# Optimization experiments

Hardware: AMD Instinct MI355X
Metric: run time of the kernel (lower is better)

Reference implementation:

```python
import jax, jax.numpy as jnp
import numpy as np

B, S, D = 16, 1024, 768          # batch, seq_len, in_features
NS, MAXW = 256, 8                # num_spans, max span width (fixed for jit)
V, C = 128, 6                    # num_vertexes, max corefs per vertex
R = 512                          # num_max_rels_per_example
REL, HID, DIS = 97, 384, 20      # relation_num, hidden_dim, dis_size
NEG = -1e30


def setup_inputs() -> dict:
    key = jax.random.key(0)
    ks = jax.random.split(key, 14)
    sentence_repr = jax.random.normal(ks[0], (B, S, D), jnp.float32)
    starts = jax.random.randint(ks[1], (B, NS), 0, S - MAXW)
    widths = jax.random.randint(ks[2], (B, NS), 0, MAXW)
    entity_span_indices = jnp.stack([starts, starts + widths], axis=-1)  # (B,NS,2), start<=end
    entity_span_indices_mask = jax.random.randint(ks[3], (B, NS), 0, 2)
    vertex_indices = jax.random.randint(ks[4], (B, V, C), 0, NS)
    vertex_indices_mask = jax.random.randint(ks[5], (B, V, C), 0, 2)
    head_tail_indices = jax.random.randint(ks[6], (B, R, 2), 0, V)
    relation_mask = jax.random.randint(ks[7], (B, R), 0, 2)
    dis_h_2_t = jax.random.randint(ks[8], (B, R), 0, 20)
    dis_t_2_h = jax.random.randint(ks[9], (B, R), 0, 20)
    dis_embed = jax.random.normal(ks[10], (20, DIS), jnp.float32) * 0.02
    dis_embed = dis_embed.at[10].set(0.0)  # padding_idx=10
    fin = D + DIS                      # final_in_features with distance
    in_proj = 2 * fin + D              # concat [head+dis, tail+dis, head*tail]
    W1 = jax.random.normal(ks[11], (in_proj, HID), jnp.float32) / np.float32(np.sqrt(in_proj))
    W2 = jax.random.normal(ks[12], (HID, REL), jnp.float32) / np.float32(np.sqrt(HID))
    b2 = jnp.zeros((REL,), jnp.float32)
    return dict(sentence_repr=sentence_repr, entity_span_indices=entity_span_indices,
                entity_span_indices_mask=entity_span_indices_mask,
                vertex_indices=vertex_indices, vertex_indices_mask=vertex_indices_mask,
                head_tail_indices=head_tail_indices, relation_mask=relation_mask,
                dis_h_2_t=dis_h_2_t, dis_t_2_h=dis_t_2_h,
                dis_embed=dis_embed, W1=W1, W2=W2, b2=b2)


def reference(sentence_repr, entity_span_indices, entity_span_indices_mask,
              vertex_indices, vertex_indices_mask, head_tail_indices,
              relation_mask, dis_h_2_t, dis_t_2_h, dis_embed, W1, W2, b2):
    Bx, Sx, Dx = sentence_repr.shape
    # --- SpanExtractor: masked max pooling over tokens in each span [start, end] ---
    starts = entity_span_indices[..., 0]
    ends = entity_span_indices[..., 1]
    pos = starts[..., None] + jnp.arange(MAXW)            # (B,NS,W)
    valid = pos <= ends[..., None]
    posc = jnp.clip(pos, 0, Sx - 1).reshape(Bx, -1)       # (B,NS*W)
    tok = jnp.take_along_axis(sentence_repr, posc[..., None], axis=1)
    tok = tok.reshape(Bx, NS, MAXW, Dx)
    span_emb = jnp.where(valid[..., None], tok, NEG).max(axis=2)   # (B,NS,D)
    # --- coref 'mean' pooling over spans per vertex (batched_index_select) ---
    vidx = vertex_indices.reshape(Bx, -1)
    ve = jnp.take_along_axis(span_emb, vidx[..., None], axis=1).reshape(Bx, V, C, Dx)
    m = vertex_indices_mask.astype(jnp.float32)
    cnt = jnp.maximum(m.sum(axis=2), 1.0)                 # num_corefs clamped >=1
    vertex_emb = (ve * m[..., None]).sum(axis=2) / cnt[..., None]  # (B,V,D)
    # --- head/tail gather ---
    hti = head_tail_indices.reshape(Bx, -1)
    ht = jnp.take_along_axis(vertex_emb, hti[..., None], axis=1).reshape(Bx, R, 2, Dx)
    head_repr = ht[:, :, 0, :]
    tail_repr = ht[:, :, 1, :]
    # (original multiplies by relation_mask and discards the result -> no-op)
    eh = dis_embed[dis_h_2_t]                              # (B,R,DIS)
    et = dis_embed[dis_t_2_h]
    feat = jnp.concatenate([head_repr, eh, tail_repr, et, head_repr * tail_repr], axis=-1)
    # TwoLayerLinear: relu(x @ W1) @ W2 + b2, bias=(False, True)
    predict_re = jax.nn.relu(feat @ W1) @ W2 + b2          # (B,R,REL)
    return predict_re
```

## Files before the change

kernel.cpp:

```cpp
#include <hip/hip_runtime.h>
#include <cstdint>
#include <cstddef>

#define B_    16
#define S_    1024
#define D_    768
#define NS_   256
#define V_    128
#define C_    6
#define R_    512
#define REL_  97
#define HID_  384
#define DIS_  20
#define K1_   2344
#define KP_   2432
#define NIT_  38
#define N2P_  128

#define BM1   128
#define BN1   64
#define SLICE_ ((size_t)8192 * HID_)

typedef unsigned short ushort_t;
typedef unsigned int   u32;
typedef short bf16x4 __attribute__((ext_vector_type(4)));
typedef short bf16x8 __attribute__((ext_vector_type(8)));
typedef float f32x4  __attribute__((ext_vector_type(4)));
typedef float f32x16 __attribute__((ext_vector_type(16)));

__device__ __forceinline__ float bf2f(short s) {
    return __uint_as_float(((unsigned int)(unsigned short)s) << 16);
}
__device__ __forceinline__ short f2bf(float x) {
    union { float f; unsigned int u; } c; c.f = x;
    unsigned int r = (c.u + 0x7fffu + ((c.u >> 16) & 1u)) >> 16;
    return (short)(unsigned short)r;
}

typedef const __attribute__((address_space(1))) u32* gas_t;
typedef __attribute__((address_space(3))) u32*       las_t;
__device__ __forceinline__ void dma16(const void* g, void* l) {
    __builtin_amdgcn_global_load_lds((gas_t)g, (las_t)l, 16, 0, 0);
}

__device__ __forceinline__ int w1_orig(int k) {
    if      (k < 768)  return k;
    else if (k < 1536) return k + 20;
    else if (k < 2304) return k + 40;
    else if (k < 2324) return 768 + (k - 2304);
    else if (k < K1_)  return 1556 + (k - 2324);
    return -1;
}

__global__ __launch_bounds__(192) void prep_kernel(
    const float* __restrict__ sr, const int* __restrict__ spans,
    const float* __restrict__ W1, const float* __restrict__ W2,
    ushort_t* __restrict__ span_emb, ushort_t* __restrict__ W1Tile,
    ushort_t* __restrict__ W2T)
{
    int blk = blockIdx.x;
    int tid = threadIdx.x;
    if (blk < 4096) {
        int bn    = blk;
        int b     = bn >> 8;
        int start = spans[2 * bn];
        int end   = spans[2 * bn + 1];
        int w     = end - start;
        const float* base = sr + ((size_t)b * S_ + start) * D_ + tid * 4;
        f32x4 x[8];
        x[0] = *(const f32x4*)base;
        switch (w) {
        case 7: x[7] = *(const f32x4*)(base + 7 * D_); [[fallthrough]];
        case 6: x[6] = *(const f32x4*)(base + 6 * D_); [[fallthrough]];
        case 5: x[5] = *(const f32x4*)(base + 5 * D_); [[fallthrough]];
        case 4: x[4] = *(const f32x4*)(base + 4 * D_); [[fallthrough]];
        case 3: x[3] = *(const f32x4*)(base + 3 * D_); [[fallthrough]];
        case 2: x[2] = *(const f32x4*)(base + 2 * D_); [[fallthrough]];
        case 1: x[1] = *(const f32x4*)(base + 1 * D_); break;
        default: break;
        }
        f32x4 m = x[0];
#pragma unroll
        for (int j = 1; j < 8; ++j)
            if (j <= w) {
#pragma unroll
                for (int c = 0; c < 4; ++c) m[c] = fmaxf(m[c], x[j][c]);
            }
        bf16x4 o;
#pragma unroll
        for (int c = 0; c < 4; ++c) o[c] = f2bf(m[c]);
        *(bf16x4*)(span_emb + (size_t)bn * D_ + tid * 4) = o;
    } else if (blk < 4096 + 608) {
        int flat = (blk - 4096) * 192 + tid;
        int nn   = flat & 63;
        int kg   = (flat >> 6) & 7;
        int itnt = flat >> 9;
        int it   = itnt / 6;
        bf16x8 p;
#pragma unroll
        for (int j = 0; j < 8; ++j) {
            int k = it * 64 + kg * 8 + j;
            int orig = w1_orig(k);
            int n    = (itnt - it * 6) * 64 + nn;
            float v = (orig >= 0) ? W1[(size_t)orig * HID_ + n] : 0.f;
            p[j] = f2bf(v);
        }
        *(bf16x8*)(W1Tile + ((size_t)itnt * 8 + kg) * 512 + nn * 8) = p;
    } else {
        int g  = (blk - 4704) * 192 + tid;
        int n  = g / 48;
        int k0 = (g - n * 48) * 8;
        bf16x8 p;
#pragma unroll
        for (int j = 0; j < 8; ++j) {
            float v = (n < REL_) ? W2[(size_t)(k0 + j) * REL_ + n] : 0.f;
            p[j] = f2bf(v);
        }
        *(bf16x8*)(W2T + (size_t)n * HID_ + k0) = p;
    }
}

__global__ __launch_bounds__(192) void vertex_kernel(
    const ushort_t* __restrict__ span_emb, const int* __restrict__ vidx,
    const int* __restrict__ vmask, ushort_t* __restrict__ vembB)
{
    int bv = blockIdx.x;
    int b  = bv >> 7;
    const int* vi = vidx  + bv * C_;
    const int* vm = vmask + bv * C_;
    int   idxs[C_];
    float ms[C_];
    float cnt = 0.f;
#pragma unroll
    for (int c = 0; c < C_; ++c) {
        idxs[c] = vi[c];
        ms[c]   = (float)vm[c];
        cnt    += ms[c];
    }
    float inv = 1.f / fmaxf(cnt, 1.f);
    int col = threadIdx.x * 4;
    float s[4] = {0.f, 0.f, 0.f, 0.f};
#pragma unroll
    for (int c = 0; c < C_; ++c) {
        if (ms[c] != 0.f) {
            bf16x4 x = *(const bf16x4*)(span_emb +
                        ((size_t)(b * NS_ + idxs[c])) * D_ + col);
#pragma unroll
            for (int q = 0; q < 4; ++q) s[q] += bf2f(x[q]);
        }
    }
    bf16x4 o;
#pragma unroll
    for (int q = 0; q < 4; ++q) o[q] = f2bf(s[q] * inv);
    *(bf16x4*)(vembB + (size_t)bv * D_ + col) = o;
}

__global__ __launch_bounds__(256, 3) void gemm1_kernel(
    const ushort_t* __restrict__ vembB, const int* __restrict__ ht,
    const int* __restrict__ dht, const int* __restrict__ dth,
    const float* __restrict__ dis, const ushort_t* __restrict__ W1Tile,
    ushort_t* __restrict__ hiddenS)
{
    __shared__ ushort_t Abuf[2][BM1][64];
    __shared__ ushort_t Bbuf[2][8][BN1][8];

    int tid  = threadIdx.x;
    int wv   = tid >> 6;
    int lane = tid & 63;
    int m0   = blockIdx.x * BM1;
    int n0   = blockIdx.y * BN1;
    int nt   = blockIdx.y;
    int ksl  = blockIdx.z;

    int rr  = lane >> 3;
    int sl  = lane & 7;
    int gsw = (sl - rr) & 7;

    int hoff[4], toff[4];
#pragma unroll
    for (int gi = 0; gi < 4; ++gi) {
        int row = wv * 32 + gi * 8 + rr;
        int g   = m0 + row;
        int b   = g >> 9;
        hoff[gi] = (b * V_ + ht[2 * g])     * D_;
        toff[gi] = (b * V_ + ht[2 * g + 1]) * D_;
    }

    auto stage = [&](int bf, int it_g) {
        int k0   = it_g * 64;
        int r    = k0 / 768;
        int koff = k0 - r * 768;
        int kk   = koff + gsw * 8;
        if (r == 0) {
#pragma unroll
            for (int gi = 0; gi < 4; ++gi)
                dma16(vembB + hoff[gi] + kk, &Abuf[bf][wv * 32 + gi * 8][0]);
        } else if (r == 1) {
#pragma unroll
            for (int gi = 0; gi < 4; ++gi)
                dma16(vembB + toff[gi] + kk, &Abuf[bf][wv * 32 + gi * 8][0]);
        } else if (r == 2) {
#pragma unroll
            for (int gi = 0; gi < 4; ++gi) {
                bf16x8 h = *(const bf16x8*)(vembB + hoff[gi] + kk);
                bf16x8 t = *(const bf16x8*)(vembB + toff[gi] + kk);
                bf16x8 p;
#pragma unroll
                for (int j = 0; j < 8; ++j) p[j] = f2bf(bf2f(h[j]) * bf2f(t[j]));
                *(bf16x8*)&Abuf[bf][wv * 32 + gi * 8 + rr][sl * 8] = p;
            }
        } else {
            int kb = k0 - 2304;
#pragma unroll
            for (int gi = 0; gi < 4; ++gi) {
                int g   = m0 + wv * 32 + gi * 8 + rr;
                int rdh = dht[g], rdt = dth[g];
                bf16x8 p;
#pragma unroll
                for (int j = 0; j < 8; ++j) {
                    int kkj = kb + gsw * 8 + j;
                    float v = 0.f;
                    if      (kkj < 20) v = dis[rdh * DIS_ + kkj];
                    else if (kkj < 40) v = dis[rdt * DIS_ + (kkj - 20)];
                    p[j] = f2bf(v);
                }
                *(bf16x8*)&Abuf[bf][wv * 32 + gi * 8 + rr][sl * 8] = p;
            }
        }
        const ushort_t* bbase = W1Tile + ((size_t)it_g * 6 + nt) * 4096;
#pragma unroll
        for (int q = 0; q < 2; ++q) {
            int p = wv * 2 + q;
            dma16(bbase + (size_t)p * 512 + lane * 8, &Bbuf[bf][p][0][0]);
        }
    };

    int half = lane >> 5;
    int lrow = lane & 31;
    int wm   = (wv & 1) * 64;
    int wn   = (wv >> 1) * 32;

    f32x16 acc[2];
#pragma unroll
    for (int i = 0; i < 2; ++i)
#pragma unroll
        for (int r = 0; r < 16; ++r) acc[i][r] = 0.f;

    stage(0, ksl);
    for (int it = 0; it < 19; ++it) {
        int bf = it & 1;
        __syncthreads();
        if (it + 1 < 19) stage(bf ^ 1, 2 * (it + 1) + ksl);
#pragma unroll
        for (int s = 0; s < 4; ++s) {
            int kg   = s * 2 + half;
            int slot = ((kg + lrow) & 7) * 8;
            bf16x8 a0 = *(bf16x8*)&Abuf[bf][wm + lrow][slot];
            bf16x8 a1 = *(bf16x8*)&Abuf[bf][wm + 32 + lrow][slot];
            bf16x8 b0 = *(bf16x8*)&Bbuf[bf][kg][wn + lrow][0];
            acc[0] = __builtin_amdgcn_mfma_f32_32x32x16_bf16(a0, b0, acc[0], 0, 0, 0);
            acc[1] = __builtin_amdgcn_mfma_f32_32x32x16_bf16(a1, b0, acc[1], 0, 0, 0);
        }
    }

    ushort_t* outp = hiddenS + (size_t)ksl * SLICE_;
    int col = n0 + wn + lrow;
#pragma unroll
    for (int fm = 0; fm < 2; ++fm) {
#pragma unroll
        for (int r = 0; r < 16; ++r) {
            int row = m0 + wm + fm * 32 + (r & 3) + 8 * (r >> 2) + 4 * half;
            outp[(size_t)row * HID_ + col] = (ushort_t)f2bf(acc[fm][r]);
        }
    }
}

__global__ __launch_bounds__(256) void gemm2_kernel(
    const ushort_t* __restrict__ hiddenS, const ushort_t* __restrict__ W2T,
    const float* __restrict__ b2, float* __restrict__ out)
{
    __shared__ ushort_t As[32][72];
    __shared__ ushort_t Bs[128][72];

    int m0  = blockIdx.x * 32;
    int tid = threadIdx.x;

    int arow = tid >> 3;
    int akk  = (tid & 7) * 8;

    bf16x8 pA; bf16x8 pB[4];
    auto loadAB = [&](int k0) {
        const ushort_t* hp = hiddenS + (size_t)(m0 + arow) * HID_ + k0 + akk;
        bf16x8 x0 = *(const bf16x8*)hp;
        bf16x8 x1 = *(const bf16x8*)(hp + SLICE_);
#pragma unroll
        for (int j = 0; j < 8; ++j)
            pA[j] = f2bf(fmaxf(bf2f(x0[j]) + bf2f(x1[j]), 0.f));
#pragma unroll
        for (int e = 0; e < 4; ++e)
            pB[e] = *(const bf16x8*)(W2T + (size_t)(arow + e * 32) * HID_ + k0 + akk);
    };

    int w    = tid >> 6;
    int lane = tid & 63;
    int wm = (w & 1) * 16;
    int wn = (w >> 1) * 64;
    int lr = lane & 15, lq = lane >> 4;

    f32x4 acc[4];
#pragma unroll
    for (int e = 0; e < 4; ++e) acc[e] = (f32x4){0.f, 0.f, 0.f, 0.f};

    loadAB(0);
    for (int k0 = 0; k0 < HID_; k0 += 64) {
        __syncthreads();
        *(bf16x8*)&As[arow][akk] = pA;
#pragma unroll
        for (int e = 0; e < 4; ++e)
            *(bf16x8*)&Bs[arow + e * 32][akk] = pB[e];
        __syncthreads();
        if (k0 + 64 < HID_) loadAB(k0 + 64);
#pragma unroll
        for (int ks = 0; ks < 2; ++ks) {
            int kb = ks * 32 + lq * 8;
            bf16x8 a = *(bf16x8*)&As[wm + lr][kb];
#pragma unroll
            for (int nf = 0; nf < 4; ++nf) {
                bf16x8 bb = *(bf16x8*)&Bs[wn + nf * 16 + lr][kb];
                acc[nf] = __builtin_amdgcn_mfma_f32_16x16x32_bf16(a, bb, acc[nf], 0, 0, 0);
            }
        }
    }

    int grow = m0 + wm + lq * 4;
#pragma unroll
    for (int nf = 0; nf < 4; ++nf) {
        int col = wn + nf * 16 + lr;
        if (col < REL_) {
            float bias = b2[col];
#pragma unroll
            for (int r = 0; r < 4; ++r)
                out[(size_t)(grow + r) * REL_ + col] = acc[nf][r] + bias;
        }
    }
}

extern "C" void kernel_launch(void* const* d_in, const int* in_sizes, int n_in,
                              void* d_out, int out_size, void* d_ws, size_t ws_size,
                              hipStream_t stream)
{
    const float* sr    = (const float*)d_in[0];
    const int*   spans = (const int*)  d_in[1];
    const int*   vidx  = (const int*)  d_in[3];
    const int*   vmask = (const int*)  d_in[4];
    const int*   ht    = (const int*)  d_in[5];
    const int*   dht   = (const int*)  d_in[7];
    const int*   dth   = (const int*)  d_in[8];
    const float* dis   = (const float*)d_in[9];
    const float* W1    = (const float*)d_in[10];
    const float* W2    = (const float*)d_in[11];
    const float* b2    = (const float*)d_in[12];
    float* out = (float*)d_out;

    ushort_t* span_emb = (ushort_t*)d_ws;
    ushort_t* vembB    = span_emb + (size_t)B_ * NS_ * D_;
    ushort_t* W1Tile   = vembB + (size_t)B_ * V_ * D_;
    ushort_t* W2T      = W1Tile + (size_t)NIT_ * 6 * 4096;
    ushort_t* hiddenS  = W2T + (size_t)N2P_ * HID_;

    prep_kernel<<<4096 + 608 + 32, 192, 0, stream>>>(
        sr, spans, W1, W2, span_emb, W1Tile, W2T);
    vertex_kernel<<<B_ * V_, 192, 0, stream>>>(span_emb, vidx, vmask, vembB);

    dim3 g1((B_ * R_) / BM1, HID_ / BN1, 2);
    gemm1_kernel<<<g1, 256, 0, stream>>>(vembB, ht, dht, dth, dis, W1Tile, hiddenS);

    gemm2_kernel<<<(B_ * R_) / 32, 256, 0, stream>>>(hiddenS, W2T, b2, out);
}
```

Before: 152.8 us.

## Split first-layer GEMM into per-vertex projections plus head*tail GEMM

The concatenated-feature GEMM is decomposed by linearity. Head and tail contributions are computed once per vertex (2048 rows) instead of once per relation (8192 rows), and the distance-embedding contributions are precomputed as small 20x384 lookup tables. Only the head*tail product block still needs a per-relation GEMM, and its epilogue gathers and adds the precomputed pieces, then applies ReLU. This removes the split-K partial buffer and its reduction in gemm2, at the cost of an extra kernel launch and fp32 gather traffic in the epilogue.

```diff
diff --git a/kernel.cpp b/kernel.cpp
--- a/kernel.cpp
+++ b/kernel.cpp
@@ -12,14 +12,8 @@
 #define REL_  97
 #define HID_  384
 #define DIS_  20
-#define K1_   2344
-#define KP_   2432
-#define NIT_  38
+#define KD_   768
 #define N2P_  128
-
-#define BM1   128
-#define BN1   64
-#define SLICE_ ((size_t)8192 * HID_)
 
 typedef unsigned short ushort_t;
 typedef unsigned int   u32;
@@ -43,20 +37,13 @@
     __builtin_amdgcn_global_load_lds((gas_t)g, (las_t)l, 16, 0, 0);
 }
 
-__device__ __forceinline__ int w1_orig(int k) {
-    if      (k < 768)  return k;
-    else if (k < 1536) return k + 20;
-    else if (k < 2304) return k + 40;
-    else if (k < 2324) return 768 + (k - 2304);
-    else if (k < K1_)  return 1556 + (k - 2324);
-    return -1;
-}
-
 __global__ __launch_bounds__(192) void prep_kernel(
     const float* __restrict__ sr, const int* __restrict__ spans,
     const float* __restrict__ W1, const float* __restrict__ W2,
-    ushort_t* __restrict__ span_emb, ushort_t* __restrict__ W1Tile,
-    ushort_t* __restrict__ W2T)
+    const float* __restrict__ dis,
+    ushort_t* __restrict__ span_emb, ushort_t* __restrict__ W1HT,
+    ushort_t* __restrict__ W1P, ushort_t* __restrict__ W2T,
+    float* __restrict__ disH, float* __restrict__ disT)
 {
     int blk = blockIdx.x;
     int tid = threadIdx.x;
@@ -90,24 +77,40 @@
 #pragma unroll
         for (int c = 0; c < 4; ++c) o[c] = f2bf(m[c]);
         *(bf16x4*)(span_emb + (size_t)bn * D_ + tid * 4) = o;
-    } else if (blk < 4096 + 608) {
+    } else if (blk < 4480) {
         int flat = (blk - 4096) * 192 + tid;
         int nn   = flat & 63;
         int kg   = (flat >> 6) & 7;
         int itnt = flat >> 9;
-        int it   = itnt / 6;
+        int it   = itnt / 12;
+        int nt   = itnt - it * 12;
         bf16x8 p;
 #pragma unroll
         for (int j = 0; j < 8; ++j) {
             int k = it * 64 + kg * 8 + j;
-            int orig = w1_orig(k);
-            int n    = (itnt - it * 6) * 64 + nn;
-            float v = (orig >= 0) ? W1[(size_t)orig * HID_ + n] : 0.f;
+            int n = nt * 64 + nn;
+            float v = (n < HID_) ? W1[(size_t)k * HID_ + n]
+                                 : W1[(size_t)(788 + k) * HID_ + (n - HID_)];
             p[j] = f2bf(v);
         }
-        *(bf16x8*)(W1Tile + ((size_t)itnt * 8 + kg) * 512 + nn * 8) = p;
-    } else {
-        int g  = (blk - 4704) * 192 + tid;
+        *(bf16x8*)(W1HT + ((size_t)itnt * 8 + kg) * 512 + nn * 8) = p;
+    } else if (blk < 4672) {
+        int flat = (blk - 4480) * 192 + tid;
+        int nn   = flat & 63;
+        int kg   = (flat >> 6) & 7;
+        int itnt = flat >> 9;
+        int it   = itnt / 6;
+        int nt   = itnt - it * 6;
+        bf16x8 p;
+#pragma unroll
+        for (int j = 0; j < 8; ++j) {
+            int k = it * 64 + kg * 8 + j;
+            int n = nt * 64 + nn;
+            p[j] = f2bf(W1[(size_t)(1576 + k) * HID_ + n]);
+        }
+        *(bf16x8*)(W1P + ((size_t)itnt * 8 + kg) * 512 + nn * 8) = p;
+    } else if (blk < 4704) {
+        int g  = (blk - 4672) * 192 + tid;
         int n  = g / 48;
         int k0 = (g - n * 48) * 8;
         bf16x8 p;
@@ -117,6 +120,18 @@
             p[j] = f2bf(v);
         }
         *(bf16x8*)(W2T + (size_t)n * HID_ + k0) = p;
+    } else {
+        int g   = (blk - 4704) * 192 + tid;
+        int sel = g >= 7680;
+        int gg  = sel ? g - 7680 : g;
+        int i   = gg / HID_;
+        int n   = gg - i * HID_;
+        int rb  = sel ? 1556 : 768;
+        float a = 0.f;
+#pragma unroll
+        for (int j = 0; j < DIS_; ++j)
+            a += dis[i * DIS_ + j] * W1[(size_t)(rb + j) * HID_ + n];
+        (sel ? disT : disH)[i * HID_ + n] = a;
     }
 }
 
@@ -155,79 +170,34 @@
     *(bf16x4*)(vembB + (size_t)bv * D_ + col) = o;
 }
 
-__global__ __launch_bounds__(256, 3) void gemm1_kernel(
-    const ushort_t* __restrict__ vembB, const int* __restrict__ ht,
-    const int* __restrict__ dht, const int* __restrict__ dth,
-    const float* __restrict__ dis, const ushort_t* __restrict__ W1Tile,
-    ushort_t* __restrict__ hiddenS)
-{
-    __shared__ ushort_t Abuf[2][BM1][64];
-    __shared__ ushort_t Bbuf[2][8][BN1][8];
+__global__ __launch_bounds__(256, 3) void gemmc_kernel(
+    const ushort_t* __restrict__ vembB, const ushort_t* __restrict__ W1HT,
+    float* __restrict__ vproj)
+{
+    __shared__ ushort_t Abuf[2][64][64];
+    __shared__ ushort_t Bbuf[2][8][64][8];
 
     int tid  = threadIdx.x;
     int wv   = tid >> 6;
     int lane = tid & 63;
-    int m0   = blockIdx.x * BM1;
-    int n0   = blockIdx.y * BN1;
+    int m0   = blockIdx.x * 64;
     int nt   = blockIdx.y;
-    int ksl  = blockIdx.z;
+    int n0   = nt * 64;
 
     int rr  = lane >> 3;
     int sl  = lane & 7;
     int gsw = (sl - rr) & 7;
 
-    int hoff[4], toff[4];
-#pragma unroll
-    for (int gi = 0; gi < 4; ++gi) {
-        int row = wv * 32 + gi * 8 + rr;
-        int g   = m0 + row;
-        int b   = g >> 9;
-        hoff[gi] = (b * V_ + ht[2 * g])     * D_;
-        toff[gi] = (b * V_ + ht[2 * g + 1]) * D_;
-    }
-
-    auto stage = [&](int bf, int it_g) {
-        int k0   = it_g * 64;
-        int r    = k0 / 768;
-        int koff = k0 - r * 768;
-        int kk   = koff + gsw * 8;
-        if (r == 0) {
-#pragma unroll
-            for (int gi = 0; gi < 4; ++gi)
-                dma16(vembB + hoff[gi] + kk, &Abuf[bf][wv * 32 + gi * 8][0]);
-        } else if (r == 1) {
-#pragma unroll
-            for (int gi = 0; gi < 4; ++gi)
-                dma16(vembB + toff[gi] + kk, &Abuf[bf][wv * 32 + gi * 8][0]);
-        } else if (r == 2) {
-#pragma unroll
-            for (int gi = 0; gi < 4; ++gi) {
-                bf16x8 h = *(const bf16x8*)(vembB + hoff[gi] + kk);
-                bf16x8 t = *(const bf16x8*)(vembB + toff[gi] + kk);
-                bf16x8 p;
-#pragma unroll
-                for (int j = 0; j < 8; ++j) p[j] = f2bf(bf2f(h[j]) * bf2f(t[j]));
-                *(bf16x8*)&Abuf[bf][wv * 32 + gi * 8 + rr][sl * 8] = p;
-            }
-        } else {
-            int kb = k0 - 2304;
-#pragma unroll
-            for (int gi = 0; gi < 4; ++gi) {
-                int g   = m0 + wv * 32 + gi * 8 + rr;
-                int rdh = dht[g], rdt = dth[g];
-                bf16x8 p;
-#pragma unroll
-                for (int j = 0; j < 8; ++j) {
-                    int kkj = kb + gsw * 8 + j;
-                    float v = 0.f;
-                    if      (kkj < 20) v = dis[rdh * DIS_ + kkj];
-                    else if (kkj < 40) v = dis[rdt * DIS_ + (kkj - 20)];
-                    p[j] = f2bf(v);
-                }
-                *(bf16x8*)&Abuf[bf][wv * 32 + gi * 8 + rr][sl * 8] = p;
-            }
-        }
-        const ushort_t* bbase = W1Tile + ((size_t)it_g * 6 + nt) * 4096;
+    const ushort_t* asrc[2];
+#pragma unroll
+    for (int gi = 0; gi < 2; ++gi)
+        asrc[gi] = vembB + (size_t)(m0 + wv * 16 + gi * 8 + rr) * KD_ + gsw * 8;
+
+    auto stage = [&](int bf, int it) {
+#pragma unroll
+        for (int gi = 0; gi < 2; ++gi)
+            dma16(asrc[gi] + it * 64, &Abuf[bf][wv * 16 + gi * 8][0]);
+        const ushort_t* bbase = W1HT + ((size_t)it * 12 + nt) * 4096;
 #pragma unroll
         for (int q = 0; q < 2; ++q) {
             int p = wv * 2 + q;
@@ -237,46 +207,134 @@
 
     int half = lane >> 5;
     int lrow = lane & 31;
-    int wm   = (wv & 1) * 64;
+    int wm   = (wv & 1) * 32;
     int wn   = (wv >> 1) * 32;
 
-    f32x16 acc[2];
-#pragma unroll
-    for (int i = 0; i < 2; ++i)
-#pragma unroll
-        for (int r = 0; r < 16; ++r) acc[i][r] = 0.f;
-
-    stage(0, ksl);
-    for (int it = 0; it < 19; ++it) {
+    f32x16 acc;
+#pragma unroll
+    for (int r = 0; r < 16; ++r) acc[r] = 0.f;
+
+    stage(0, 0);
+    for (int it = 0; it < 12; ++it) {
         int bf = it & 1;
         __syncthreads();
-        if (it + 1 < 19) stage(bf ^ 1, 2 * (it + 1) + ksl);
+        if (it + 1 < 12) stage(bf ^ 1, it + 1);
 #pragma unroll
         for (int s = 0; s < 4; ++s) {
             int kg   = s * 2 + half;
             int slot = ((kg + lrow) & 7) * 8;
-            bf16x8 a0 = *(bf16x8*)&Abuf[bf][wm + lrow][slot];
-            bf16x8 a1 = *(bf16x8*)&Abuf[bf][wm + 32 + lrow][slot];
-            bf16x8 b0 = *(bf16x8*)&Bbuf[bf][kg][wn + lrow][0];
-            acc[0] = __builtin_amdgcn_mfma_f32_32x32x16_bf16(a0, b0, acc[0], 0, 0, 0);
-            acc[1] = __builtin_amdgcn_mfma_f32_32x32x16_bf16(a1, b0, acc[1], 0, 0, 0);
-        }
-    }
-
-    ushort_t* outp = hiddenS + (size_t)ksl * SLICE_;
+            bf16x8 a = *(bf16x8*)&Abuf[bf][wm + lrow][slot];
+            bf16x8 b = *(bf16x8*)&Bbuf[bf][kg][wn + lrow][0];
+            acc = __builtin_amdgcn_mfma_f32_32x32x16_bf16(a, b, acc, 0, 0, 0);
+        }
+    }
+
     int col = n0 + wn + lrow;
 #pragma unroll
-    for (int fm = 0; fm < 2; ++fm) {
-#pragma unroll
-        for (int r = 0; r < 16; ++r) {
-            int row = m0 + wm + fm * 32 + (r & 3) + 8 * (r >> 2) + 4 * half;
-            outp[(size_t)row * HID_ + col] = (ushort_t)f2bf(acc[fm][r]);
-        }
+    for (int r = 0; r < 16; ++r) {
+        int row = m0 + wm + (r & 3) + 8 * (r >> 2) + 4 * half;
+        vproj[(size_t)row * KD_ + col] = acc[r];
+    }
+}
+
+__global__ __launch_bounds__(256, 3) void gemmd_kernel(
+    const ushort_t* __restrict__ vembB, const int* __restrict__ ht,
+    const int* __restrict__ dht, const int* __restrict__ dth,
+    const ushort_t* __restrict__ W1P, const float* __restrict__ vproj,
+    const float* __restrict__ disH, const float* __restrict__ disT,
+    ushort_t* __restrict__ hidden)
+{
+    __shared__ ushort_t Abuf[2][64][64];
+    __shared__ ushort_t Bbuf[2][8][64][8];
+    __shared__ int hI[64], tI[64], dhI[64], dtI[64];
+
+    int tid  = threadIdx.x;
+    int wv   = tid >> 6;
+    int lane = tid & 63;
+    int m0   = blockIdx.x * 64;
+    int nt   = blockIdx.y;
+    int n0   = nt * 64;
+
+    int rr  = lane >> 3;
+    int sl  = lane & 7;
+    int gsw = (sl - rr) & 7;
+
+    if (tid < 64) {
+        int g = m0 + tid;
+        int b = g >> 9;
+        hI[tid]  = b * V_ + ht[2 * g];
+        tI[tid]  = b * V_ + ht[2 * g + 1];
+        dhI[tid] = dht[g];
+        dtI[tid] = dth[g];
+    }
+
+    int hoff[2], toff[2];
+#pragma unroll
+    for (int gi = 0; gi < 2; ++gi) {
+        int g = m0 + wv * 16 + gi * 8 + rr;
+        int b = g >> 9;
+        hoff[gi] = (b * V_ + ht[2 * g])     * KD_;
+        toff[gi] = (b * V_ + ht[2 * g + 1]) * KD_;
+    }
+
+    auto stage = [&](int bf, int it) {
+        int kk = it * 64 + gsw * 8;
+#pragma unroll
+        for (int gi = 0; gi < 2; ++gi) {
+            bf16x8 h = *(const bf16x8*)(vembB + hoff[gi] + kk);
+            bf16x8 t = *(const bf16x8*)(vembB + toff[gi] + kk);
+            bf16x8 p;
+#pragma unroll
+            for (int j = 0; j < 8; ++j) p[j] = f2bf(bf2f(h[j]) * bf2f(t[j]));
+            *(bf16x8*)&Abuf[bf][wv * 16 + gi * 8 + rr][sl * 8] = p;
+        }
+        const ushort_t* bbase = W1P + ((size_t)it * 6 + nt) * 4096;
+#pragma unroll
+        for (int q = 0; q < 2; ++q) {
+            int p = wv * 2 + q;
+            dma16(bbase + (size_t)p * 512 + lane * 8, &Bbuf[bf][p][0][0]);
+        }
+    };
+
+    int half = lane >> 5;
+    int lrow = lane & 31;
+    int wm   = (wv & 1) * 32;
+    int wn   = (wv >> 1) * 32;
+
+    f32x16 acc;
+#pragma unroll
+    for (int r = 0; r < 16; ++r) acc[r] = 0.f;
+
+    stage(0, 0);
+    for (int it = 0; it < 12; ++it) {
+        int bf = it & 1;
+        __syncthreads();
+        if (it + 1 < 12) stage(bf ^ 1, it + 1);
+#pragma unroll
+        for (int s = 0; s < 4; ++s) {
+            int kg   = s * 2 + half;
+            int slot = ((kg + lrow) & 7) * 8;
+            bf16x8 a = *(bf16x8*)&Abuf[bf][wm + lrow][slot];
+            bf16x8 b = *(bf16x8*)&Bbuf[bf][kg][wn + lrow][0];
+            acc = __builtin_amdgcn_mfma_f32_32x32x16_bf16(a, b, acc, 0, 0, 0);
+        }
+    }
+
+    int col = n0 + wn + lrow;
+#pragma unroll
+    for (int r = 0; r < 16; ++r) {
+        int rl = wm + (r & 3) + 8 * (r >> 2) + 4 * half;
+        float v = acc[r]
+                + vproj[(size_t)hI[rl] * KD_ + col]
+                + vproj[(size_t)tI[rl] * KD_ + HID_ + col]
+                + disH[dhI[rl] * HID_ + col]
+                + disT[dtI[rl] * HID_ + col];
+        hidden[(size_t)(m0 + rl) * HID_ + col] = (ushort_t)f2bf(fmaxf(v, 0.f));
     }
 }
 
 __global__ __launch_bounds__(256) void gemm2_kernel(
-    const ushort_t* __restrict__ hiddenS, const ushort_t* __restrict__ W2T,
+    const ushort_t* __restrict__ hidden, const ushort_t* __restrict__ W2T,
     const float* __restrict__ b2, float* __restrict__ out)
 {
     __shared__ ushort_t As[32][72];
@@ -290,12 +348,7 @@
 
     bf16x8 pA; bf16x8 pB[4];
     auto loadAB = [&](int k0) {
-        const ushort_t* hp = hiddenS + (size_t)(m0 + arow) * HID_ + k0 + akk;
-        bf16x8 x0 = *(const bf16x8*)hp;
-        bf16x8 x1 = *(const bf16x8*)(hp + SLICE_);
-#pragma unroll
-        for (int j = 0; j < 8; ++j)
-            pA[j] = f2bf(fmaxf(bf2f(x0[j]) + bf2f(x1[j]), 0.f));
+        pA = *(const bf16x8*)(hidden + (size_t)(m0 + arow) * HID_ + k0 + akk);
 #pragma unroll
         for (int e = 0; e < 4; ++e)
             pB[e] = *(const bf16x8*)(W2T + (size_t)(arow + e * 32) * HID_ + k0 + akk);
@@ -364,16 +417,21 @@
 
     ushort_t* span_emb = (ushort_t*)d_ws;
     ushort_t* vembB    = span_emb + (size_t)B_ * NS_ * D_;
-    ushort_t* W1Tile   = vembB + (size_t)B_ * V_ * D_;
-    ushort_t* W2T      = W1Tile + (size_t)NIT_ * 6 * 4096;
-    ushort_t* hiddenS  = W2T + (size_t)N2P_ * HID_;
-
-    prep_kernel<<<4096 + 608 + 32, 192, 0, stream>>>(
-        sr, spans, W1, W2, span_emb, W1Tile, W2T);
+    ushort_t* W1HT     = vembB + (size_t)B_ * V_ * D_;
+    ushort_t* W1P      = W1HT + (size_t)144 * 4096;
+    ushort_t* W2T      = W1P + (size_t)72 * 4096;
+    ushort_t* hidden   = W2T + (size_t)N2P_ * HID_;
+    float* vproj = (float*)(hidden + (size_t)B_ * R_ * HID_);
+    float* disH  = vproj + (size_t)B_ * V_ * KD_;
+    float* disT  = disH + (size_t)DIS_ * HID_;
+
+    prep_kernel<<<4784, 192, 0, stream>>>(
+        sr, spans, W1, W2, dis, span_emb, W1HT, W1P, W2T, disH, disT);
     vertex_kernel<<<B_ * V_, 192, 0, stream>>>(span_emb, vidx, vmask, vembB);
 
-    dim3 g1((B_ * R_) / BM1, HID_ / BN1, 2);
-    gemm1_kernel<<<g1, 256, 0, stream>>>(vembB, ht, dht, dth, dis, W1Tile, hiddenS);
-
-    gemm2_kernel<<<(B_ * R_) / 32, 256, 0, stream>>>(hiddenS, W2T, b2, out);
-}
+    gemmc_kernel<<<dim3(32, 12), 256, 0, stream>>>(vembB, W1HT, vproj);
+    gemmd_kernel<<<dim3(128, 6), 256, 0, stream>>>(
+        vembB, ht, dht, dth, W1P, vproj, disH, disT, hidden);
+
+    gemm2_kernel<<<(B_ * R_) / 32, 256, 0, stream>>>(hidden, W2T, b2, out);
+}
```

Measured after the change: 151.6 us. About the same (-0.8%).
